# Optimization experiments

Measured on AMD Instinct MI355X. Metric: run time of the kernel, lower is better.

## Reference

```python
import jax, jax.numpy as jnp
import numpy as np

B, C_IN, N = 8, 512, 4096   # batch, input channels, timesteps
D, K = 256, 2048            # code dim (n_out), codebook size (vq_n_embed)
EMA_G = 0.99                # vq_ema_gamma


def setup_inputs() -> dict:
    key = jax.random.key(0)
    k1, k2, k3 = jax.random.split(key, 3)
    z = jax.random.normal(k1, (B, C_IN, N), jnp.float32)
    # emb: xavier_uniform with gain=10 over (K, D)
    eb = 10.0 * np.sqrt(6.0 / (K + D))
    emb = jax.random.uniform(k2, (K, D), jnp.float32, -eb, eb)
    # 1x1 Conv1d weight (no bias), xavier_uniform over (D, C_IN)
    wb = np.sqrt(6.0 / (D + C_IN))
    W = jax.random.uniform(k3, (D, C_IN), jnp.float32, -wb, wb)
    # EMA buffers as initialized in __init__
    ema_numer = emb * (1.0 - EMA_G)
    ema_denom = jnp.ones((K,), jnp.float32) * (1.0 - EMA_G)
    return {"z": z, "W": W, "emb": emb, "ema_numer": ema_numer, "ema_denom": ema_denom}


def reference(z, W, emb, ema_numer, ema_denom):
    # 1x1 conv (no bias): ze (B, D, N)
    ze = jnp.einsum('dc,bcn->bdn', W, z)
    e = jax.lax.stop_gradient(emb)  # sg(emb)
    # Squared L2 distances (B, K, N) via ||ze||^2 + ||e||^2 - 2 e.ze
    # (mathematically equal to the broadcasted (ze-e)^2 sum, without the
    #  huge (B,K,D,N) intermediate)
    ze_sq = jnp.sum(ze * ze, axis=1)              # (B, N)
    e_sq = jnp.sum(e * e, axis=1)                 # (K,)
    cross = jnp.einsum('kd,bdn->bkn', e, ze)      # (B, K, N)
    d2 = ze_sq[:, None, :] + e_sq[None, :, None] - 2.0 * cross
    min_ind = jnp.argmin(d2, axis=1)              # (B, N) int
    zq = jnp.take(e, min_ind, axis=0).transpose(0, 2, 1)  # (B, D, N)
    # ReplaceGrad straight-through: value = zq, gradient flows to ze
    out = ze + jax.lax.stop_gradient(zq - ze)
    # EMA codebook statistics (scatter-add over assignments)
    flat_ind = min_ind.reshape(-1)                          # (B*N,)
    flat_ze = ze.transpose(0, 2, 1).reshape(-1, D)          # (B*N, D)
    z_sum = jax.ops.segment_sum(flat_ze, flat_ind, num_segments=K)
    n_sum = jax.ops.segment_sum(jnp.ones((flat_ind.shape[0],), ze.dtype), flat_ind, num_segments=K)
    ema_numer_new = EMA_G * ema_numer + (1.0 - EMA_G) * z_sum
    ema_denom_new = EMA_G * ema_denom + (1.0 - EMA_G) * n_sum
    return out, ema_numer_new, ema_denom_new
```

## Files before the change

### kernel.cpp

```cpp
#include <hip/hip_runtime.h>

#define B_   8
#define CIN  512
#define NN_  4096
#define DD   256
#define KK   2048
#define KSPLIT 4
#define KPER (KK / KSPLIT)
#define NG   (B_ * NN_)

typedef _Float16 f16x8 __attribute__((ext_vector_type(8)));
typedef _Float16 f16x4 __attribute__((ext_vector_type(4)));
typedef float    f32x16 __attribute__((ext_vector_type(16)));

#define MFMA16 __builtin_amdgcn_mfma_f32_32x32x16_f16

#define GLDS16(gp, lp) __builtin_amdgcn_global_load_lds( \
    (const __attribute__((address_space(1))) void*)(gp), \
    (__attribute__((address_space(3))) void*)(lp), 16, 0, 0)

__device__ __forceinline__ unsigned ford(float f) {
  unsigned u = __float_as_uint(f);
  return (u & 0x80000000u) ? ~u : (u | 0x80000000u);
}

__global__ __launch_bounds__(256) void k_init0(const float* __restrict__ emb,
                                               const float* __restrict__ ema_numer,
                                               float* __restrict__ esq,
                                               _Float16* __restrict__ emb_h,
                                               _Float16* __restrict__ emb_l,
                                               float* __restrict__ out_numer,
                                               unsigned* __restrict__ mind64w,
                                               int* __restrict__ hist,
                                               int* __restrict__ done) {
  const int bid = blockIdx.x;
  const int t = threadIdx.x;
  if (bid < KK / 4) {
    int lane = t & 63;
    int k = bid * 4 + (t >> 6);
    float4 v = *(const float4*)&emb[(size_t)k * DD + 4 * lane];
    float s = v.x * v.x + v.y * v.y + v.z * v.z + v.w * v.w;
    f16x4 h, l;
    float* vp = (float*)&v;
#pragma unroll
    for (int i = 0; i < 4; i++) {
      _Float16 hh = (_Float16)vp[i];
      h[i] = hh;
      l[i] = (_Float16)(vp[i] - (float)hh);
    }
    *(f16x4*)&emb_h[(size_t)k * DD + 4 * lane] = h;
    *(f16x4*)&emb_l[(size_t)k * DD + 4 * lane] = l;
    for (int off = 32; off > 0; off >>= 1) s += __shfl_down(s, off, 64);
    if (lane == 0) esq[k] = s;
  } else {
    int i = (bid - KK / 4) * 256 + t;
    if (i < KK * DD) out_numer[i] = 0.99f * ema_numer[i];
    else {
      int j = i - KK * DD;
      if (j < 2 * NG) mind64w[j] = 0xFFFFFFFFu;
      else if (j < 2 * NG + KK) hist[j - 2 * NG] = 0;
      else done[j - 2 * NG - KK] = 0;
    }
  }
}

__global__ __launch_bounds__(256) void k_ze(const float* __restrict__ W,
                                            const float* __restrict__ z,
                                            _Float16* __restrict__ zeT_h,
                                            _Float16* __restrict__ zeT_l) {
  __shared__ __align__(16) char sm[69632];
  const int t = threadIdx.x;
  const int w = t >> 6, lane = t & 63;
  const int lr = lane & 31, lh = lane >> 5;
  const int wm = w & 1, wn = w >> 1;
  const int swz = (lr >> 1) & 3;
  const int b = blockIdx.z, d0 = blockIdx.y * 128, n0 = blockIdx.x * 128;

  auto stageA = [&](int buf, int c0) {
    _Float16* Ah = (_Float16*)(sm + buf * 8192);
    _Float16* Al = (_Float16*)(sm + 16384 + buf * 8192);
#pragma unroll
    for (int i = 0; i < 4; i++) {
      int fid = i * 256 + t;
      int d = fid >> 3, q8 = fid & 7;
      float4 v = *(const float4*)&W[(size_t)(d0 + d) * CIN + c0 + 4 * q8];
      float* vp = (float*)&v;
      f16x4 h, l;
#pragma unroll
      for (int e = 0; e < 4; e++) {
        _Float16 hh = (_Float16)vp[e];
        h[e] = hh;
        l[e] = (_Float16)(vp[e] - (float)hh);
      }
      int p16 = (q8 >> 1) ^ ((d >> 1) & 3);
      int off = d * 32 + p16 * 8 + (q8 & 1) * 4;
      *(f16x4*)&Ah[off] = h;
      *(f16x4*)&Al[off] = l;
    }
  };

  auto stageZ = [&](int buf, int c0) {
    const int n_l = t & 127, cg = t >> 7;
    const float* gp = z + ((size_t)b * CIN + c0 + cg * 16) * NN_ + n0 + n_l;
    float v[16];
#pragma unroll
    for (int j = 0; j < 16; j++) v[j] = gp[(size_t)j * NN_];
    _Float16* Zh = (_Float16*)(sm + 32768 + buf * 8192);
    _Float16* Zl = (_Float16*)(sm + 49152 + buf * 8192);
#pragma unroll
    for (int q = 0; q < 2; q++) {
      f16x8 h, l;
#pragma unroll
      for (int e = 0; e < 8; e++) {
        float x = v[q * 8 + e];
        _Float16 hh = (_Float16)x;
        h[e] = hh;
        l[e] = (_Float16)(x - (float)hh);
      }
      int p = (cg * 2 + q) ^ ((n_l >> 1) & 3);
      *(f16x8*)&Zh[n_l * 32 + p * 8] = h;
      *(f16x8*)&Zl[n_l * 32 + p * 8] = l;
    }
  };

  f32x16 acc[2][2];
#pragma unroll
  for (int mt = 0; mt < 2; mt++)
#pragma unroll
    for (int nt = 0; nt < 2; nt++)
#pragma unroll
      for (int i = 0; i < 16; i++) acc[mt][nt][i] = 0.0f;

  stageA(0, 0);
  stageZ(0, 0);
  int buf = 0;
  for (int c0 = 0; c0 < CIN; c0 += 32) {
    __syncthreads();
    if (c0 + 32 < CIN) { stageA(buf ^ 1, c0 + 32); stageZ(buf ^ 1, c0 + 32); }
    const _Float16* WhB = (const _Float16*)(sm + buf * 8192);
    const _Float16* WlB = (const _Float16*)(sm + 16384 + buf * 8192);
    const _Float16* ZhB = (const _Float16*)(sm + 32768 + buf * 8192);
    const _Float16* ZlB = (const _Float16*)(sm + 49152 + buf * 8192);
#pragma unroll
    for (int s = 0; s < 2; s++) {
      const int p = (2 * s + lh) ^ swz;
      const int acol = p * 8;
      const int ar0 = (wm * 64 + lr) * 32 + acol;
      const int ar1 = (wm * 64 + 32 + lr) * 32 + acol;
      const int br0 = (wn * 64 + lr) * 32 + acol;
      const int br1 = (wn * 64 + 32 + lr) * 32 + acol;
      f16x8 ah0 = *(const f16x8*)(WhB + ar0);
      f16x8 ah1 = *(const f16x8*)(WhB + ar1);
      f16x8 al0 = *(const f16x8*)(WlB + ar0);
      f16x8 al1 = *(const f16x8*)(WlB + ar1);
      f16x8 bh0 = *(const f16x8*)(ZhB + br0);
      f16x8 bh1 = *(const f16x8*)(ZhB + br1);
      f16x8 bl0 = *(const f16x8*)(ZlB + br0);
      f16x8 bl1 = *(const f16x8*)(ZlB + br1);
      acc[0][0] = MFMA16(ah0, bh0, acc[0][0], 0, 0, 0);
      acc[0][1] = MFMA16(ah0, bh1, acc[0][1], 0, 0, 0);
      acc[1][0] = MFMA16(ah1, bh0, acc[1][0], 0, 0, 0);
      acc[1][1] = MFMA16(ah1, bh1, acc[1][1], 0, 0, 0);
      acc[0][0] = MFMA16(ah0, bl0, acc[0][0], 0, 0, 0);
      acc[0][1] = MFMA16(ah0, bl1, acc[0][1], 0, 0, 0);
      acc[1][0] = MFMA16(ah1, bl0, acc[1][0], 0, 0, 0);
      acc[1][1] = MFMA16(ah1, bl1, acc[1][1], 0, 0, 0);
      acc[0][0] = MFMA16(al0, bh0, acc[0][0], 0, 0, 0);
      acc[0][1] = MFMA16(al0, bh1, acc[0][1], 0, 0, 0);
      acc[1][0] = MFMA16(al1, bh0, acc[1][0], 0, 0, 0);
      acc[1][1] = MFMA16(al1, bh1, acc[1][1], 0, 0, 0);
    }
    buf ^= 1;
  }

  __syncthreads();
  _Float16* Eh = (_Float16*)sm;
  _Float16* El = (_Float16*)(sm + 33792);
#pragma unroll
  for (int mt = 0; mt < 2; mt++)
#pragma unroll
    for (int nt = 0; nt < 2; nt++) {
      int n_l = wn * 64 + nt * 32 + lr;
#pragma unroll
      for (int g = 0; g < 4; g++) {
        int d_l = wm * 64 + mt * 32 + 8 * g + 4 * lh;
        f16x4 h, l;
#pragma unroll
        for (int e = 0; e < 4; e++) {
          float x = acc[mt][nt][4 * g + e];
          _Float16 hh = (_Float16)x;
          h[e] = hh;
          l[e] = (_Float16)(x - (float)hh);
        }
        *(f16x4*)&Eh[n_l * 132 + d_l] = h;
        *(f16x4*)&El[n_l * 132 + d_l] = l;
      }
    }
  __syncthreads();
  _Float16* gh = zeT_h + ((size_t)b * NN_ + n0) * DD + d0;
  _Float16* gl = zeT_l + ((size_t)b * NN_ + n0) * DD + d0;
#pragma unroll
  for (int i = 0; i < 16; i++) {
    int n = i * 8 + w * 2 + lh;
    int d = 4 * lr;
    *(f16x4*)&gh[(size_t)n * DD + d] = *(const f16x4*)&Eh[n * 132 + d];
    *(f16x4*)&gl[(size_t)n * DD + d] = *(const f16x4*)&El[n * 132 + d];
  }
}

__global__ __launch_bounds__(256) void k_argmin(const _Float16* __restrict__ emb_h,
                                                const _Float16* __restrict__ emb_l,
                                                const _Float16* __restrict__ zeT_h,
                                                const _Float16* __restrict__ zeT_l,
                                                const float* __restrict__ esq,
                                                unsigned long long* __restrict__ mind64) {
  __shared__ __align__(16) char sm[69632];
  const int t = threadIdx.x;
  const int w = t >> 6, lane = t & 63;
  const int lr = lane & 31, lh = lane >> 5;
  const int wm = w & 1, wn = w >> 1;
  const int swz = (lr >> 1) & 3;
  const int b = blockIdx.y, n0 = blockIdx.x * 128, ks = blockIdx.z;
  const int kbase = ks * KPER;

  float* esqs = (float*)(sm + 65536);
  *(float2*)&esqs[2 * t] = *(const float2*)&esq[kbase + 2 * t];

  const _Float16* zb_h = zeT_h + ((size_t)b * NN_ + n0) * DD;
  const _Float16* zb_l = zeT_l + ((size_t)b * NN_ + n0) * DD;

  auto stage = [&](int buf, int kt, int dc) {
    const int k0 = kbase + kt * 128;
    const int q = lane & 3, rr = lane >> 2;
    const int g = q ^ ((rr >> 1) & 3);
    const int rb0 = 32 * w;
#pragma unroll
    for (int j = 0; j < 2; j++) {
      int rb = rb0 + 16 * j;
      int r = rb + rr;
      int col = dc + 8 * g;
      size_t eo = (size_t)(k0 + r) * DD + col;
      size_t zo = (size_t)r * DD + col;
      char* lb = sm + (size_t)buf * 8192 + rb * 64;
      GLDS16(emb_h + eo, lb);
      GLDS16(emb_l + eo, lb + 16384);
      GLDS16(zb_h + zo, lb + 32768);
      GLDS16(zb_l + zo, lb + 49152);
    }
  };

  f32x16 vzero;
#pragma unroll
  for (int i = 0; i < 16; i++) vzero[i] = 0.0f;

  float bestv[2];
  int   besti[2];
  bestv[0] = bestv[1] = 3.4e38f;
  besti[0] = besti[1] = 0;

  stage(0, 0, 0);
  int buf = 0;
  for (int kt = 0; kt < 4; kt++) {
    f32x16 acc00 = vzero, acc01 = vzero, acc10 = vzero, acc11 = vzero;
    for (int dc = 0; dc < DD; dc += 32) {
      __syncthreads();
      if (dc + 32 < DD) stage(buf ^ 1, kt, dc + 32);
      else if (kt < 3) stage(buf ^ 1, kt + 1, 0);
      const _Float16* EHb = (const _Float16*)(sm + buf * 8192);
      const _Float16* ELb = (const _Float16*)(sm + 16384 + buf * 8192);
      const _Float16* ZHb = (const _Float16*)(sm + 32768 + buf * 8192);
      const _Float16* ZLb = (const _Float16*)(sm + 49152 + buf * 8192);
#pragma unroll
      for (int s = 0; s < 2; s++) {
        const int p = (2 * s + lh) ^ swz;
        const int acol = p * 8;
        const int ar0 = (wm * 64 + lr) * 32 + acol;
        const int ar1 = (wm * 64 + 32 + lr) * 32 + acol;
        const int br0 = (wn * 64 + lr) * 32 + acol;
        const int br1 = (wn * 64 + 32 + lr) * 32 + acol;
        f16x8 ah0 = *(const f16x8*)(EHb + ar0);
        f16x8 ah1 = *(const f16x8*)(EHb + ar1);
        f16x8 al0 = *(const f16x8*)(ELb + ar0);
        f16x8 al1 = *(const f16x8*)(ELb + ar1);
        f16x8 bh0 = *(const f16x8*)(ZHb + br0);
        f16x8 bh1 = *(const f16x8*)(ZHb + br1);
        f16x8 bl0 = *(const f16x8*)(ZLb + br0);
        f16x8 bl1 = *(const f16x8*)(ZLb + br1);
        acc00 = MFMA16(ah0, bh0, acc00, 0, 0, 0);
        acc01 = MFMA16(ah0, bh1, acc01, 0, 0, 0);
        acc10 = MFMA16(ah1, bh0, acc10, 0, 0, 0);
        acc11 = MFMA16(ah1, bh1, acc11, 0, 0, 0);
        acc00 = MFMA16(ah0, bl0, acc00, 0, 0, 0);
        acc01 = MFMA16(ah0, bl1, acc01, 0, 0, 0);
        acc10 = MFMA16(ah1, bl0, acc10, 0, 0, 0);
        acc11 = MFMA16(ah1, bl1, acc11, 0, 0, 0);
        acc00 = MFMA16(al0, bh0, acc00, 0, 0, 0);
        acc01 = MFMA16(al0, bh1, acc01, 0, 0, 0);
        acc10 = MFMA16(al1, bh0, acc10, 0, 0, 0);
        acc11 = MFMA16(al1, bh1, acc11, 0, 0, 0);
      }
      buf ^= 1;
    }
#pragma unroll
    for (int mt = 0; mt < 2; mt++)
#pragma unroll
      for (int nt = 0; nt < 2; nt++) {
        const f32x16& a = (mt == 0) ? (nt == 0 ? acc00 : acc01)
                                    : (nt == 0 ? acc10 : acc11);
#pragma unroll
        for (int r = 0; r < 16; r++) {
          int kl = kt * 128 + wm * 64 + mt * 32 + (r & 3) + 8 * (r >> 2) + 4 * lh;
          float d2 = esqs[kl] - 2.0f * a[r];
          int kg = kbase + kl;
          if (d2 < bestv[nt] || (d2 == bestv[nt] && kg < besti[nt])) {
            bestv[nt] = d2; besti[nt] = kg;
          }
        }
      }
  }

#pragma unroll
  for (int nt = 0; nt < 2; nt++) {
    float ov = __shfl_xor(bestv[nt], 32, 64);
    int   oi = __shfl_xor(besti[nt], 32, 64);
    if (ov < bestv[nt] || (ov == bestv[nt] && oi < besti[nt])) {
      bestv[nt] = ov; besti[nt] = oi;
    }
  }
  float* pv = (float*)(sm + 67584);
  int*   pi = (int*)(sm + 68608);
  __syncthreads();
  if (lh == 0) {
#pragma unroll
    for (int nt = 0; nt < 2; nt++) {
      pv[(w * 2 + nt) * 32 + lr] = bestv[nt];
      pi[(w * 2 + nt) * 32 + lr] = besti[nt];
    }
  }
  __syncthreads();
  if (t < 128) {
    int wn2 = t >> 6, nt = (t >> 5) & 1, nl = t & 31;
    int i0 = ((2 * wn2 + 0) * 2 + nt) * 32 + nl;
    int i1 = ((2 * wn2 + 1) * 2 + nt) * 32 + nl;
    float v0 = pv[i0], v1 = pv[i1];
    int   j0 = pi[i0], j1 = pi[i1];
    if (v1 < v0 || (v1 == v0 && j1 < j0)) { v0 = v1; j0 = j1; }
    unsigned long long pk = ((unsigned long long)ford(v0) << 32) | (unsigned)j0;
    atomicMin(&mind64[(size_t)b * NN_ + n0 + t], pk);
  }
}

__global__ __launch_bounds__(256) void k_scan(const unsigned long long* __restrict__ mind64,
                                              const float* __restrict__ ema_denom,
                                              int* __restrict__ hist,
                                              int* __restrict__ done,
                                              int* __restrict__ cursor,
                                              float* __restrict__ out_denom) {
  __shared__ int h[KK];
  __shared__ int ps[256];
  __shared__ int lastFlag;
  const int t = threadIdx.x;
#pragma unroll
  for (int i = 0; i < 8; i++) h[t + 256 * i] = 0;
  __syncthreads();
  const int base = blockIdx.x * (NG / 16);
#pragma unroll
  for (int i = 0; i < NG / 16 / 256; i++) {
    int idx = (int)(mind64[base + i * 256 + t] & 0xFFFFFFFFULL);
    atomicAdd(&h[idx], 1);
  }
  __syncthreads();
#pragma unroll
  for (int i = 0; i < 8; i++) {
    int v = h[t + 256 * i];
    if (v) atomicAdd(&hist[t + 256 * i], v);
  }
  __threadfence();
  __syncthreads();
  if (t == 0) lastFlag = (atomicAdd(done, 1) == 15);
  __syncthreads();
  if (!lastFlag) return;

  int c[8], s = 0;
#pragma unroll
  for (int e = 0; e < 8; e++) { c[e] = atomicAdd(&hist[8 * t + e], 0); s += c[e]; }
  ps[t] = s;
  __syncthreads();
  for (int off = 1; off < 256; off <<= 1) {
    int v = (t >= off) ? ps[t - off] : 0;
    __syncthreads();
    ps[t] += v;
    __syncthreads();
  }
  int run = ps[t] - s;
#pragma unroll
  for (int e = 0; e < 8; e++) {
    cursor[8 * t + e] = run;
    out_denom[8 * t + e] = 0.99f * ema_denom[8 * t + e]
                         + 0.009999999776482582f * (float)c[e];
    run += c[e];
  }
}

__global__ __launch_bounds__(256) void k_out(const float* __restrict__ emb,
                                             const unsigned long long* __restrict__ mind64,
                                             float* __restrict__ out,
                                             int* __restrict__ cursor,
                                             int* __restrict__ sortp) {
  __shared__ __align__(16) float E[64][257];
  __shared__ int idxl[64];
  const int t = threadIdx.x;
  const int b  = blockIdx.y;
  const int n0 = blockIdx.x * 64;
  if (t < 64) idxl[t] = (int)(mind64[(size_t)b * NN_ + n0 + t] & 0xFFFFFFFFULL);
  __syncthreads();

  if (t < 64) {
    int g = b * NN_ + n0 + t;
    int k = idxl[t];
    int p = atomicAdd(&cursor[k], 1);
    sortp[p] = (k << 15) | g;
  }

  for (int i = 0; i < 16; i++) {
    int cid = t + 256 * i;
    int r = cid >> 6, q = cid & 63;
    float4 v = *(const float4*)&emb[(size_t)idxl[r] * DD + 4 * q];
    float* vp = (float*)&v;
    E[r][4 * q + 0] = vp[0];
    E[r][4 * q + 1] = vp[1];
    E[r][4 * q + 2] = vp[2];
    E[r][4 * q + 3] = vp[3];
  }
  __syncthreads();
  const int nq = t & 15, dg = t >> 4;
  float* outb = out + (size_t)b * DD * NN_ + n0;
#pragma unroll
  for (int i = 0; i < 16; i++) {
    int d = i * 16 + dg;
    float4 v = make_float4(E[4 * nq + 0][d], E[4 * nq + 1][d],
                           E[4 * nq + 2][d], E[4 * nq + 3][d]);
    *(float4*)&outb[(size_t)d * NN_ + 4 * nq] = v;
  }
}

__global__ __launch_bounds__(256) void k_zsum(const int* __restrict__ sortp,
                                              const _Float16* __restrict__ zeT_h,
                                              const _Float16* __restrict__ zeT_l,
                                              float* __restrict__ out_numer) {
  const float OG = 0.009999999776482582f;
  __shared__ int sg[256];
  const int t = threadIdx.x;
  const int w = t >> 6, lane = t & 63;
  sg[t] = sortp[blockIdx.x * 256 + t];
  __syncthreads();
  const int base = w * 64;
  float acc[4] = {0.f, 0.f, 0.f, 0.f};
  int cur = sg[base] >> 15;
  for (int j = 0; j < 64; j++) {
    int e = sg[base + j];
    int k = e >> 15, g = e & 32767;
    if (k != cur) {
      float* zs = &out_numer[(size_t)cur * DD + 4 * lane];
#pragma unroll
      for (int x = 0; x < 4; x++) { atomicAdd(&zs[x], OG * acc[x]); acc[x] = 0.f; }
      cur = k;
    }
    f16x4 h = *(const f16x4*)&zeT_h[(size_t)g * DD + 4 * lane];
    f16x4 l = *(const f16x4*)&zeT_l[(size_t)g * DD + 4 * lane];
#pragma unroll
    for (int x = 0; x < 4; x++) acc[x] += (float)h[x] + (float)l[x];
  }
  float* zs = &out_numer[(size_t)cur * DD + 4 * lane];
#pragma unroll
  for (int x = 0; x < 4; x++) atomicAdd(&zs[x], OG * acc[x]);
}

extern "C" void kernel_launch(void* const* d_in, const int* in_sizes, int n_in,
                              void* d_out, int out_size, void* d_ws, size_t ws_size,
                              hipStream_t stream) {
  (void)in_sizes; (void)n_in; (void)out_size; (void)ws_size;
  const float* z         = (const float*)d_in[0];
  const float* W         = (const float*)d_in[1];
  const float* emb       = (const float*)d_in[2];
  const float* ema_numer = (const float*)d_in[3];
  const float* ema_denom = (const float*)d_in[4];

  float* out       = (float*)d_out;
  float* out_numer = out + (size_t)B_ * DD * NN_;
  float* out_denom = out_numer + (size_t)KK * DD;

  const size_t ZET = (size_t)B_ * NN_ * DD;
  _Float16* zeT_h = (_Float16*)d_ws;
  _Float16* zeT_l = zeT_h + ZET;
  float* esq    = (float*)(zeT_l + ZET);
  int*   cursor = (int*)(esq + KK);
  int*   sortp  = cursor + KK;
  unsigned long long* mind64 = (unsigned long long*)(sortp + NG);
  int*   hist   = (int*)(mind64 + NG);
  int*   done   = hist + KK;
  _Float16* emb_h = (_Float16*)(done + 256);
  _Float16* emb_l = emb_h + (size_t)KK * DD;

  const int initBlocks = KK / 4 + (KK * DD + 2 * NG + KK + 256) / 256;
  k_init0<<<dim3(initBlocks), 256, 0, stream>>>(emb, ema_numer, esq, emb_h, emb_l,
                                                out_numer, (unsigned*)mind64, hist, done);
  k_ze<<<dim3(NN_ / 128, DD / 128, B_), 256, 0, stream>>>(W, z, zeT_h, zeT_l);
  k_argmin<<<dim3(NN_ / 128, B_, KSPLIT), 256, 0, stream>>>(emb_h, emb_l, zeT_h, zeT_l,
                                                            esq, mind64);
  k_scan<<<dim3(16), 256, 0, stream>>>(mind64, ema_denom, hist, done, cursor, out_denom);
  k_out<<<dim3(NN_ / 64, B_), 256, 0, stream>>>(emb, mind64, out, cursor, sortp);
  k_zsum<<<dim3(NG / 256), 256, 0, stream>>>(sortp, zeT_h, zeT_l, out_numer);
}
```

Measured before the change: 292.7 us.

## Merge init into ze kernel and fuse tail into one cooperative kernel

```diff
diff --git a/kernel.cpp b/kernel.cpp
--- a/kernel.cpp
+++ b/kernel.cpp
@@ -1,4 +1,7 @@
 #include <hip/hip_runtime.h>
+#include <hip/hip_cooperative_groups.h>
+
+namespace cg = cooperative_groups;
 
 #define B_   8
 #define CIN  512
@@ -24,57 +27,57 @@
   return (u & 0x80000000u) ? ~u : (u | 0x80000000u);
 }
 
-__global__ __launch_bounds__(256) void k_init0(const float* __restrict__ emb,
-                                               const float* __restrict__ ema_numer,
-                                               float* __restrict__ esq,
-                                               _Float16* __restrict__ emb_h,
-                                               _Float16* __restrict__ emb_l,
-                                               float* __restrict__ out_numer,
-                                               unsigned* __restrict__ mind64w,
-                                               int* __restrict__ hist,
-                                               int* __restrict__ done) {
+__global__ __launch_bounds__(256) void k_pre(const float* __restrict__ W,
+                                             const float* __restrict__ z,
+                                             _Float16* __restrict__ zeT_h,
+                                             _Float16* __restrict__ zeT_l,
+                                             const float* __restrict__ emb,
+                                             const float* __restrict__ ema_numer,
+                                             float* __restrict__ esq,
+                                             _Float16* __restrict__ emb_h,
+                                             _Float16* __restrict__ emb_l,
+                                             float* __restrict__ out_numer,
+                                             unsigned* __restrict__ mind64w,
+                                             int* __restrict__ hist) {
+  __shared__ __align__(16) char sm[69632];
   const int bid = blockIdx.x;
   const int t = threadIdx.x;
-  if (bid < KK / 4) {
-    int lane = t & 63;
-    int k = bid * 4 + (t >> 6);
-    float4 v = *(const float4*)&emb[(size_t)k * DD + 4 * lane];
-    float s = v.x * v.x + v.y * v.y + v.z * v.z + v.w * v.w;
-    f16x4 h, l;
-    float* vp = (float*)&v;
-#pragma unroll
-    for (int i = 0; i < 4; i++) {
-      _Float16 hh = (_Float16)vp[i];
-      h[i] = hh;
-      l[i] = (_Float16)(vp[i] - (float)hh);
-    }
-    *(f16x4*)&emb_h[(size_t)k * DD + 4 * lane] = h;
-    *(f16x4*)&emb_l[(size_t)k * DD + 4 * lane] = l;
-    for (int off = 32; off > 0; off >>= 1) s += __shfl_down(s, off, 64);
-    if (lane == 0) esq[k] = s;
-  } else {
-    int i = (bid - KK / 4) * 256 + t;
-    if (i < KK * DD) out_numer[i] = 0.99f * ema_numer[i];
-    else {
-      int j = i - KK * DD;
-      if (j < 2 * NG) mind64w[j] = 0xFFFFFFFFu;
-      else if (j < 2 * NG + KK) hist[j - 2 * NG] = 0;
-      else done[j - 2 * NG - KK] = 0;
-    }
-  }
-}
-
-__global__ __launch_bounds__(256) void k_ze(const float* __restrict__ W,
-                                            const float* __restrict__ z,
-                                            _Float16* __restrict__ zeT_h,
-                                            _Float16* __restrict__ zeT_l) {
-  __shared__ __align__(16) char sm[69632];
-  const int t = threadIdx.x;
+
+  if (bid >= 512) {
+    if (bid < 1024) {
+      int lane = t & 63;
+      int k = (bid - 512) * 4 + (t >> 6);
+      float4 v = *(const float4*)&emb[(size_t)k * DD + 4 * lane];
+      float s = v.x * v.x + v.y * v.y + v.z * v.z + v.w * v.w;
+      f16x4 h, l;
+      float* vp = (float*)&v;
+#pragma unroll
+      for (int i = 0; i < 4; i++) {
+        _Float16 hh = (_Float16)vp[i];
+        h[i] = hh;
+        l[i] = (_Float16)(vp[i] - (float)hh);
+      }
+      *(f16x4*)&emb_h[(size_t)k * DD + 4 * lane] = h;
+      *(f16x4*)&emb_l[(size_t)k * DD + 4 * lane] = l;
+      for (int off = 32; off > 0; off >>= 1) s += __shfl_down(s, off, 64);
+      if (lane == 0) esq[k] = s;
+    } else {
+      int i = (bid - 1024) * 256 + t;
+      if (i < KK * DD) out_numer[i] = 0.99f * ema_numer[i];
+      else {
+        int j = i - KK * DD;
+        if (j < 2 * NG) mind64w[j] = 0xFFFFFFFFu;
+        else if (j < 2 * NG + KK) hist[j - 2 * NG] = 0;
+      }
+    }
+    return;
+  }
+
   const int w = t >> 6, lane = t & 63;
   const int lr = lane & 31, lh = lane >> 5;
   const int wm = w & 1, wn = w >> 1;
   const int swz = (lr >> 1) & 3;
-  const int b = blockIdx.z, d0 = blockIdx.y * 128, n0 = blockIdx.x * 128;
+  const int b = bid >> 6, d0 = ((bid >> 5) & 1) * 128, n0 = (bid & 31) * 128;
 
   auto stageA = [&](int buf, int c0) {
     _Float16* Ah = (_Float16*)(sm + buf * 8192);
@@ -100,8 +103,8 @@
   };
 
   auto stageZ = [&](int buf, int c0) {
-    const int n_l = t & 127, cg = t >> 7;
-    const float* gp = z + ((size_t)b * CIN + c0 + cg * 16) * NN_ + n0 + n_l;
+    const int n_l = t & 127, cg2 = t >> 7;
+    const float* gp = z + ((size_t)b * CIN + c0 + cg2 * 16) * NN_ + n0 + n_l;
     float v[16];
 #pragma unroll
     for (int j = 0; j < 16; j++) v[j] = gp[(size_t)j * NN_];
@@ -117,7 +120,7 @@
         h[e] = hh;
         l[e] = (_Float16)(x - (float)hh);
       }
-      int p = (cg * 2 + q) ^ ((n_l >> 1) & 3);
+      int p = (cg2 * 2 + q) ^ ((n_l >> 1) & 3);
       *(f16x8*)&Zh[n_l * 32 + p * 8] = h;
       *(f16x8*)&Zl[n_l * 32 + p * 8] = l;
     }
@@ -350,130 +353,112 @@
   }
 }
 
-__global__ __launch_bounds__(256) void k_scan(const unsigned long long* __restrict__ mind64,
+__global__ __launch_bounds__(256) void k_tail(const float* __restrict__ emb,
+                                              const unsigned long long* __restrict__ mind64,
                                               const float* __restrict__ ema_denom,
                                               int* __restrict__ hist,
-                                              int* __restrict__ done,
                                               int* __restrict__ cursor,
-                                              float* __restrict__ out_denom) {
-  __shared__ int h[KK];
-  __shared__ int ps[256];
-  __shared__ int lastFlag;
-  const int t = threadIdx.x;
-#pragma unroll
-  for (int i = 0; i < 8; i++) h[t + 256 * i] = 0;
-  __syncthreads();
-  const int base = blockIdx.x * (NG / 16);
-#pragma unroll
-  for (int i = 0; i < NG / 16 / 256; i++) {
-    int idx = (int)(mind64[base + i * 256 + t] & 0xFFFFFFFFULL);
-    atomicAdd(&h[idx], 1);
-  }
-  __syncthreads();
-#pragma unroll
-  for (int i = 0; i < 8; i++) {
-    int v = h[t + 256 * i];
-    if (v) atomicAdd(&hist[t + 256 * i], v);
-  }
-  __threadfence();
-  __syncthreads();
-  if (t == 0) lastFlag = (atomicAdd(done, 1) == 15);
-  __syncthreads();
-  if (!lastFlag) return;
-
-  int c[8], s = 0;
-#pragma unroll
-  for (int e = 0; e < 8; e++) { c[e] = atomicAdd(&hist[8 * t + e], 0); s += c[e]; }
-  ps[t] = s;
-  __syncthreads();
-  for (int off = 1; off < 256; off <<= 1) {
-    int v = (t >= off) ? ps[t - off] : 0;
-    __syncthreads();
-    ps[t] += v;
-    __syncthreads();
-  }
-  int run = ps[t] - s;
-#pragma unroll
-  for (int e = 0; e < 8; e++) {
-    cursor[8 * t + e] = run;
-    out_denom[8 * t + e] = 0.99f * ema_denom[8 * t + e]
-                         + 0.009999999776482582f * (float)c[e];
-    run += c[e];
-  }
-}
-
-__global__ __launch_bounds__(256) void k_out(const float* __restrict__ emb,
-                                             const unsigned long long* __restrict__ mind64,
-                                             float* __restrict__ out,
-                                             int* __restrict__ cursor,
-                                             int* __restrict__ sortp) {
+                                              int* __restrict__ sortp,
+                                              float* __restrict__ out,
+                                              float* __restrict__ out_denom,
+                                              const _Float16* __restrict__ zeT_h,
+                                              const _Float16* __restrict__ zeT_l,
+                                              float* __restrict__ out_numer) {
+  cg::grid_group grid = cg::this_grid();
   __shared__ __align__(16) float E[64][257];
   __shared__ int idxl[64];
   const int t = threadIdx.x;
-  const int b  = blockIdx.y;
-  const int n0 = blockIdx.x * 64;
-  if (t < 64) idxl[t] = (int)(mind64[(size_t)b * NN_ + n0 + t] & 0xFFFFFFFFULL);
-  __syncthreads();
+  const int g = blockIdx.x;
+  const int b = g >> 6;
+  const int n0 = (g & 63) * 64;
 
   if (t < 64) {
-    int g = b * NN_ + n0 + t;
-    int k = idxl[t];
-    int p = atomicAdd(&cursor[k], 1);
-    sortp[p] = (k << 15) | g;
-  }
-
+    int k = (int)(mind64[(size_t)b * NN_ + n0 + t] & 0xFFFFFFFFULL);
+    idxl[t] = k;
+    atomicAdd(&hist[k], 1);
+  }
+  __syncthreads();
   for (int i = 0; i < 16; i++) {
     int cid = t + 256 * i;
     int r = cid >> 6, q = cid & 63;
     float4 v = *(const float4*)&emb[(size_t)idxl[r] * DD + 4 * q];
-    float* vp = (float*)&v;
-    E[r][4 * q + 0] = vp[0];
-    E[r][4 * q + 1] = vp[1];
-    E[r][4 * q + 2] = vp[2];
-    E[r][4 * q + 3] = vp[3];
-  }
-  __syncthreads();
-  const int nq = t & 15, dg = t >> 4;
-  float* outb = out + (size_t)b * DD * NN_ + n0;
-#pragma unroll
-  for (int i = 0; i < 16; i++) {
-    int d = i * 16 + dg;
-    float4 v = make_float4(E[4 * nq + 0][d], E[4 * nq + 1][d],
-                           E[4 * nq + 2][d], E[4 * nq + 3][d]);
-    *(float4*)&outb[(size_t)d * NN_ + 4 * nq] = v;
-  }
-}
-
-__global__ __launch_bounds__(256) void k_zsum(const int* __restrict__ sortp,
-                                              const _Float16* __restrict__ zeT_h,
-                                              const _Float16* __restrict__ zeT_l,
-                                              float* __restrict__ out_numer) {
-  const float OG = 0.009999999776482582f;
-  __shared__ int sg[256];
-  const int t = threadIdx.x;
-  const int w = t >> 6, lane = t & 63;
-  sg[t] = sortp[blockIdx.x * 256 + t];
-  __syncthreads();
-  const int base = w * 64;
-  float acc[4] = {0.f, 0.f, 0.f, 0.f};
-  int cur = sg[base] >> 15;
-  for (int j = 0; j < 64; j++) {
-    int e = sg[base + j];
-    int k = e >> 15, g = e & 32767;
-    if (k != cur) {
-      float* zs = &out_numer[(size_t)cur * DD + 4 * lane];
-#pragma unroll
-      for (int x = 0; x < 4; x++) { atomicAdd(&zs[x], OG * acc[x]); acc[x] = 0.f; }
-      cur = k;
-    }
-    f16x4 h = *(const f16x4*)&zeT_h[(size_t)g * DD + 4 * lane];
-    f16x4 l = *(const f16x4*)&zeT_l[(size_t)g * DD + 4 * lane];
-#pragma unroll
-    for (int x = 0; x < 4; x++) acc[x] += (float)h[x] + (float)l[x];
-  }
-  float* zs = &out_numer[(size_t)cur * DD + 4 * lane];
-#pragma unroll
-  for (int x = 0; x < 4; x++) atomicAdd(&zs[x], OG * acc[x]);
+    E[r][4 * q + 0] = v.x;
+    E[r][4 * q + 1] = v.y;
+    E[r][4 * q + 2] = v.z;
+    E[r][4 * q + 3] = v.w;
+  }
+  __syncthreads();
+  {
+    const int nq = t & 15, dg = t >> 4;
+    float* outb = out + (size_t)b * DD * NN_ + n0;
+#pragma unroll
+    for (int i = 0; i < 16; i++) {
+      int d = i * 16 + dg;
+      float4 v = make_float4(E[4 * nq + 0][d], E[4 * nq + 1][d],
+                             E[4 * nq + 2][d], E[4 * nq + 3][d]);
+      *(float4*)&outb[(size_t)d * NN_ + 4 * nq] = v;
+    }
+  }
+  grid.sync();
+
+  if (g == 0) {
+    int* ps = (int*)&E[0][0];
+    int c[8], s = 0;
+#pragma unroll
+    for (int e = 0; e < 8; e++) { c[e] = atomicAdd(&hist[8 * t + e], 0); s += c[e]; }
+    ps[t] = s;
+    __syncthreads();
+    for (int off = 1; off < 256; off <<= 1) {
+      int v = (t >= off) ? ps[t - off] : 0;
+      __syncthreads();
+      ps[t] += v;
+      __syncthreads();
+    }
+    int run = ps[t] - s;
+#pragma unroll
+    for (int e = 0; e < 8; e++) {
+      cursor[8 * t + e] = run;
+      out_denom[8 * t + e] = 0.99f * ema_denom[8 * t + e]
+                           + 0.009999999776482582f * (float)c[e];
+      run += c[e];
+    }
+  }
+  grid.sync();
+
+  if (t < 64) {
+    int k = idxl[t];
+    int p = atomicAdd(&cursor[k], 1);
+    sortp[p] = (k << 15) | (b * NN_ + n0 + t);
+  }
+  grid.sync();
+
+  if (g < 128) {
+    const float OG = 0.009999999776482582f;
+    int* sg = (int*)&E[0][0];
+    const int w = t >> 6, lane = t & 63;
+    sg[t] = sortp[g * 256 + t];
+    __syncthreads();
+    const int base = w * 64;
+    float acc[4] = {0.f, 0.f, 0.f, 0.f};
+    int cur = sg[base] >> 15;
+    for (int j = 0; j < 64; j++) {
+      int e = sg[base + j];
+      int k = e >> 15, gi = e & 32767;
+      if (k != cur) {
+        float* zs = &out_numer[(size_t)cur * DD + 4 * lane];
+#pragma unroll
+        for (int x = 0; x < 4; x++) { atomicAdd(&zs[x], OG * acc[x]); acc[x] = 0.f; }
+        cur = k;
+      }
+      f16x4 h = *(const f16x4*)&zeT_h[(size_t)gi * DD + 4 * lane];
+      f16x4 l = *(const f16x4*)&zeT_l[(size_t)gi * DD + 4 * lane];
+#pragma unroll
+      for (int x = 0; x < 4; x++) acc[x] += (float)h[x] + (float)l[x];
+    }
+    float* zs = &out_numer[(size_t)cur * DD + 4 * lane];
+#pragma unroll
+    for (int x = 0; x < 4; x++) atomicAdd(&zs[x], OG * acc[x]);
+  }
 }
 
 extern "C" void kernel_launch(void* const* d_in, const int* in_sizes, int n_in,
@@ -498,17 +483,17 @@
   int*   sortp  = cursor + KK;
   unsigned long long* mind64 = (unsigned long long*)(sortp + NG);
   int*   hist   = (int*)(mind64 + NG);
-  int*   done   = hist + KK;
-  _Float16* emb_h = (_Float16*)(done + 256);
+  _Float16* emb_h = (_Float16*)(hist + KK);
   _Float16* emb_l = emb_h + (size_t)KK * DD;
 
-  const int initBlocks = KK / 4 + (KK * DD + 2 * NG + KK + 256) / 256;
-  k_init0<<<dim3(initBlocks), 256, 0, stream>>>(emb, ema_numer, esq, emb_h, emb_l,
-                                                out_numer, (unsigned*)mind64, hist, done);
-  k_ze<<<dim3(NN_ / 128, DD / 128, B_), 256, 0, stream>>>(W, z, zeT_h, zeT_l);
+  const int preBlocks = 1024 + (KK * DD + 2 * NG + KK) / 256;
+  k_pre<<<dim3(preBlocks), 256, 0, stream>>>(W, z, zeT_h, zeT_l, emb, ema_numer,
+                                             esq, emb_h, emb_l, out_numer,
+                                             (unsigned*)mind64, hist);
   k_argmin<<<dim3(NN_ / 128, B_, KSPLIT), 256, 0, stream>>>(emb_h, emb_l, zeT_h, zeT_l,
                                                             esq, mind64);
-  k_scan<<<dim3(16), 256, 0, stream>>>(mind64, ema_denom, hist, done, cursor, out_denom);
-  k_out<<<dim3(NN_ / 64, B_), 256, 0, stream>>>(emb, mind64, out, cursor, sortp);
-  k_zsum<<<dim3(NG / 256), 256, 0, stream>>>(sortp, zeT_h, zeT_l, out_numer);
+  void* targs[] = {(void*)&emb, (void*)&mind64, (void*)&ema_denom, (void*)&hist,
+                   (void*)&cursor, (void*)&sortp, (void*)&out, (void*)&out_denom,
+                   (void*)&zeT_h, (void*)&zeT_l, (void*)&out_numer};
+  hipLaunchCooperativeKernel((void*)k_tail, dim3(512), dim3(256), targs, 0, stream);
 }
```

Result: slower. 473.5 us (+61.8%).
